# Performance work log

Hardware: AMD Instinct MI355X
Metric: run time of the kernel (lower is better)

Reference implementation:

```python
import jax, jax.numpy as jnp
import numpy as np

B = 16384       # batch size
NT = 26         # number of embedding tables
NROWS = 100000  # rows per table
M = 128         # embedding dim == bottom MLP output dim
BOT = [13, 512, 256, 128]
TOP = [479, 1024, 1024, 512, 256, 1]


def _linear_params(k, n, m):
    kw, kb = jax.random.split(k)
    W = jax.random.normal(kw, (m, n), jnp.float32) * np.sqrt(2.0 / (m + n))
    b = jax.random.normal(kb, (m,), jnp.float32) * np.sqrt(1.0 / m)
    return W, b


def setup_inputs() -> dict:
    key = jax.random.key(0)
    ks = jax.random.split(key, 16)
    dense_x = jax.random.normal(ks[0], (B, 13), jnp.float32)
    lS_i = jax.random.randint(ks[1], (NT, B), 0, NROWS, dtype=jnp.int32)
    lS_o = jnp.tile(jnp.arange(B, dtype=jnp.int32), (NT, 1))  # 1 index per bag
    s = float(np.sqrt(1.0 / NROWS))
    emb = jax.random.uniform(ks[2], (NT, NROWS, M), jnp.float32, -s, s)
    d = {"dense_x": dense_x, "lS_o": lS_o, "lS_i": lS_i, "emb": emb}
    for i in range(3):
        W, b = _linear_params(ks[3 + i], BOT[i], BOT[i + 1])
        d[f"bw{i}"] = W; d[f"bb{i}"] = b
    for i in range(5):
        W, b = _linear_params(ks[6 + i], TOP[i], TOP[i + 1])
        d[f"tw{i}"] = W; d[f"tb{i}"] = b
    return d


def _emb_bag_sum(table, idx, off):
    # nn.EmbeddingBag(mode='sum'): bag k sums rows idx[off[k]:off[k+1]]
    L = idx.shape[0]
    bag = jnp.searchsorted(off, jnp.arange(L, dtype=off.dtype), side='right') - 1
    return jax.ops.segment_sum(table[idx], bag, num_segments=B)  # [B, M]


def _forward(dense_x, emb, bws, bbs, tws, tbs, lS_o, lS_i):
    # bottom MLP (all ReLU, sigmoid_bot=-1)
    x = dense_x
    for W, b in zip(bws, bbs):
        x = jax.nn.relu(x @ W.T + b)
    # multi-table embedding-bag sum pooling
    ly = jax.vmap(_emb_bag_sum)(emb, lS_i, lS_o)          # [NT, B, M]
    # dot interaction
    T = jnp.concatenate([x[None], ly], axis=0).transpose(1, 0, 2)  # [B, NT+1, M]
    Z = jnp.einsum('bim,bjm->bij', T, T)                  # [B, 27, 27]
    li, lj = jnp.tril_indices(NT + 1, k=-1)               # pairs i>j, torch order
    Zflat = Z[:, li, lj]                                  # [B, 351]
    z = jnp.concatenate([x, Zflat], axis=1)               # [B, 479]
    # top MLP: ReLU except Sigmoid at layer index 4 (sigmoid_top=4)
    for i, (W, b) in enumerate(zip(tws, tbs)):
        z = z @ W.T + b
        z = jax.nn.sigmoid(z) if i == 4 else jax.nn.relu(z)
    return z


def reference(dense_x, lS_o, lS_i, emb,
              bw0, bb0, bw1, bb1, bw2, bb2,
              tw0, tb0, tw1, tb1, tw2, tb2, tw3, tb3, tw4, tb4):
    return _forward(dense_x, emb,
                    [bw0, bw1, bw2], [bb0, bb1, bb2],
                    [tw0, tw1, tw2, tw3, tw4], [tb0, tb1, tb2, tb3, tb4],
                    lS_o, lS_i)
```

## Files before the change

### kernel.cpp

```cpp
#include <hip/hip_runtime.h>
#include <cstdint>
#include <cstddef>

typedef _Float16 h16;
typedef __attribute__((ext_vector_type(8))) _Float16 half8;
typedef __attribute__((ext_vector_type(4))) _Float16 half4;
typedef __attribute__((ext_vector_type(2))) _Float16 half2v;
typedef __attribute__((ext_vector_type(4))) float f32x4;
typedef __attribute__((ext_vector_type(2))) float f32x2;

#define NB 16384
#define NTAB 26
#define NR 100000

__device__ __forceinline__ void gload16(const void* g, void* l) {
  __builtin_amdgcn_global_load_lds(
      (const __attribute__((address_space(1))) unsigned int*)g,
      (__attribute__((address_space(3))) unsigned int*)l, 16, 0, 0);
}

__global__ __launch_bounds__(256) void cvt_bot0_k(
    const float* __restrict__ s0, const float* __restrict__ s1,
    const float* __restrict__ s2, const float* __restrict__ s3,
    const float* __restrict__ s4, const float* __restrict__ s5,
    h16* __restrict__ dst, const float* __restrict__ x,
    const float* __restrict__ W0, const float* __restrict__ b0,
    h16* __restrict__ Y) {
  __shared__ float xs[32][14];
  int b = blockIdx.x;
  if (b >= 9344) {
    const int bb = b - 9344;
    const int row0 = bb * 32;
    const int tid = threadIdx.x;
    for (int i = tid; i < 32 * 13; i += 256) {
      int r = i / 13, k = i - r * 13;
      xs[r][k] = x[(size_t)(row0 + r) * 13 + k];
    }
    float w0[13], w1[13];
#pragma unroll
    for (int k = 0; k < 13; ++k) {
      w0[k] = W0[tid * 13 + k];
      w1[k] = W0[(tid + 256) * 13 + k];
    }
    const float bz0 = b0[tid], bz1 = b0[tid + 256];
    __syncthreads();
    for (int r = 0; r < 32; ++r) {
      float a0 = bz0, a1 = bz1;
#pragma unroll
      for (int k = 0; k < 13; ++k) {
        const float xv = xs[r][k];
        a0 += xv * w0[k];
        a1 += xv * w1[k];
      }
      Y[(size_t)(row0 + r) * 512 + tid] = (h16)fmaxf(a0, 0.f);
      Y[(size_t)(row0 + r) * 512 + tid + 256] = (h16)fmaxf(a1, 0.f);
    }
    return;
  }
  const float* src; int K, kl, i0; size_t doff;
  if (b < 512)       { src=s0; K=512;  kl=9;  i0=(b-0)*256;    doff=0; }
  else if (b < 640)  { src=s1; K=256;  kl=8;  i0=(b-512)*256;  doff=131072; }
  else if (b < 2688) { src=s2; K=479;  kl=9;  i0=(b-640)*256;  doff=163840; }
  else if (b < 6784) { src=s3; K=1024; kl=10; i0=(b-2688)*256; doff=688128; }
  else if (b < 8832) { src=s4; K=1024; kl=10; i0=(b-6784)*256; doff=1736704; }
  else               { src=s5; K=512;  kl=9;  i0=(b-8832)*256; doff=2260992; }
  int i = i0 + threadIdx.x;
  int n = i >> kl, k = i & ((1 << kl) - 1);
  dst[doff + i] = (k < K) ? (h16)src[(size_t)n * K + k] : (h16)0.f;
}

__global__ __launch_bounds__(256, 2) void mid_k(
    const h16* __restrict__ Y0, const h16* __restrict__ W1,
    const float* __restrict__ b1, const h16* __restrict__ W2,
    const float* __restrict__ b2, h16* __restrict__ Xc) {
  __shared__ __align__(16) h16 Sa[64 * 64];
  __shared__ __align__(16) h16 Sb[256 * 64];
  __shared__ __align__(16) h16 Y1[64 * 264];
  const int tid = threadIdx.x;
  const int lane = tid & 63;
  const int w = tid >> 6;
  const int l15 = lane & 15;
  const int kq = lane >> 4;
  const int l7 = lane & 7;
  const int lr8 = lane >> 3;
  const size_t row0 = (size_t)blockIdx.x * 64;

  const int sch = (lane & 7) ^ lr8;
  const h16* gA = Y0 + (row0 + w * 16 + lr8) * 512 + sch * 8;
  const h16* gB = W1 + ((size_t)w * 64 + lr8) * 512 + sch * 8;

  f32x4 acc[4][4] = {};
  for (int t = 0; t < 8; ++t) {
    const int k0 = t * 64;
#pragma unroll
    for (int i = 0; i < 2; ++i)
      gload16(gA + (size_t)i * 8 * 512 + k0, Sa + w * 1024 + i * 512);
#pragma unroll
    for (int i = 0; i < 8; ++i)
      gload16(gB + (size_t)i * 8 * 512 + k0, Sb + w * 4096 + i * 512);
    __syncthreads();
#pragma unroll
    for (int kk = 0; kk < 2; ++kk) {
      const int kb = kk * 4 + kq;
      half8 a[4], bfr[4];
#pragma unroll
      for (int mi = 0; mi < 4; ++mi)
        a[mi] = *(const half8*)&Sa[(mi * 16 + l15) * 64 + ((kb ^ l7) << 3)];
#pragma unroll
      for (int ni = 0; ni < 4; ++ni)
        bfr[ni] = *(const half8*)&Sb[(w * 64 + ni * 16 + l15) * 64 + ((kb ^ l7) << 3)];
#pragma unroll
      for (int mi = 0; mi < 4; ++mi)
#pragma unroll
        for (int ni = 0; ni < 4; ++ni)
          acc[mi][ni] = __builtin_amdgcn_mfma_f32_16x16x32_f16(bfr[ni], a[mi], acc[mi][ni], 0, 0, 0);
    }
    __syncthreads();
  }

#pragma unroll
  for (int mi = 0; mi < 4; ++mi) {
    const int row = mi * 16 + l15;
#pragma unroll
    for (int ni = 0; ni < 4; ++ni) {
      const int col = w * 64 + ni * 16 + kq * 4;
      const f32x4 bv = *(const f32x4*)&b1[col];
      half4 h;
#pragma unroll
      for (int ri = 0; ri < 4; ++ri)
        h[ri] = (h16)fmaxf(acc[mi][ni][ri] + bv[ri], 0.f);
      *(half4*)&Y1[row * 264 + col] = h;
    }
  }
  __syncthreads();

  f32x4 acc2[4][2] = {};
  for (int ks = 0; ks < 8; ++ks) {
    half8 av[4], bv[2];
#pragma unroll
    for (int mi = 0; mi < 4; ++mi)
      av[mi] = *(const half8*)&Y1[(mi * 16 + l15) * 264 + ks * 32 + kq * 8];
#pragma unroll
    for (int nf = 0; nf < 2; ++nf) {
      const int col = (w * 2 + nf) * 16 + l15;
      bv[nf] = *(const half8*)&W2[(size_t)col * 256 + ks * 32 + kq * 8];
    }
#pragma unroll
    for (int mi = 0; mi < 4; ++mi)
#pragma unroll
      for (int nf = 0; nf < 2; ++nf)
        acc2[mi][nf] = __builtin_amdgcn_mfma_f32_16x16x32_f16(bv[nf], av[mi], acc2[mi][nf], 0, 0, 0);
  }
#pragma unroll
  for (int mi = 0; mi < 4; ++mi) {
    const size_t row = row0 + mi * 16 + l15;
#pragma unroll
    for (int nf = 0; nf < 2; ++nf) {
      const int col = (w * 2 + nf) * 16 + kq * 4;
      const f32x4 bv = *(const f32x4*)&b2[col];
      half4 h;
#pragma unroll
      for (int ri = 0; ri < 4; ++ri)
        h[ri] = (h16)fmaxf(acc2[mi][nf][ri] + bv[ri], 0.f);
      *(half4*)&Xc[row * 128 + col] = h;
    }
  }
}

template <int GYL>
__global__ __launch_bounds__(256, 4) void gemm_sb(
    const h16* __restrict__ A, const h16* __restrict__ W,
    const float* __restrict__ bias, h16* __restrict__ C, int N, int K) {
  __shared__ __align__(16) h16 As[128 * 64];
  __shared__ __align__(16) h16 Bs[128 * 64];
  const int b = blockIdx.x;
  const int c8 = b & 7;
  const int q = b >> 3;
  const int jcol = q & ((1 << GYL) - 1);
  const int krow = ((q >> GYL) << 3) | c8;
  const int tid = threadIdx.x;
  const int lane = tid & 63;
  const int wave = tid >> 6;
  const int wm = wave >> 1, wn = wave & 1;
  const size_t row0 = (size_t)krow * 128;
  const size_t col0 = (size_t)jcol * 128;
  const int lr = lane >> 3;
  const int swzc = (((lane & 7) ^ lr) << 3);
  const int l15 = lane & 15;
  const int kq = lane >> 4;
  const int l7 = lane & 7;
  const int nt = K >> 6;

  const h16* ga = A + (row0 + wave * 32 + lr) * (size_t)K + swzc;
  const h16* gb = W + (col0 + wave * 32 + lr) * (size_t)K + swzc;

  f32x4 acc[4][4] = {};

  for (int t = 0; t < nt; ++t) {
    const int k0 = t << 6;
    h16* la = As + wave * 2048;
    h16* lb = Bs + wave * 2048;
#pragma unroll
    for (int i = 0; i < 4; ++i) {
      gload16(ga + (size_t)i * 8 * K + k0, la + i * 512);
      gload16(gb + (size_t)i * 8 * K + k0, lb + i * 512);
    }
    __syncthreads();
#pragma unroll
    for (int kk = 0; kk < 2; ++kk) {
      half8 a[4], bfr[4];
      const int kb = kk * 4 + kq;
#pragma unroll
      for (int mi = 0; mi < 4; ++mi)
        a[mi] = *(const half8*)&As[(wm * 64 + mi * 16 + l15) * 64 + ((kb ^ l7) << 3)];
#pragma unroll
      for (int ni = 0; ni < 4; ++ni)
        bfr[ni] = *(const half8*)&Bs[(wn * 64 + ni * 16 + l15) * 64 + ((kb ^ l7) << 3)];
#pragma unroll
      for (int mi = 0; mi < 4; ++mi)
#pragma unroll
        for (int ni = 0; ni < 4; ++ni)
          acc[mi][ni] = __builtin_amdgcn_mfma_f32_16x16x32_f16(a[mi], bfr[ni], acc[mi][ni], 0, 0, 0);
    }
    __syncthreads();
  }

#pragma unroll
  for (int mi = 0; mi < 4; ++mi)
#pragma unroll
    for (int ni = 0; ni < 4; ++ni) {
      const size_t col = col0 + wn * 64 + ni * 16 + l15;
      const float bv = bias[col];
#pragma unroll
      for (int ri = 0; ri < 4; ++ri) {
        const size_t row = row0 + wm * 64 + mi * 16 + kq * 4 + ri;
        float v = acc[mi][ni][ri] + bv;
        C[row * N + col] = (h16)fmaxf(v, 0.f);
      }
    }
}

__global__ __launch_bounds__(256, 4) void gemm_t3f(
    const h16* __restrict__ A, const h16* __restrict__ W,
    const float* __restrict__ bias, const float* __restrict__ w4,
    float* __restrict__ partial) {
  const int K = 512;
  __shared__ __align__(16) h16 As[128 * 64];
  __shared__ __align__(16) h16 Bs[128 * 64];
  const int b = blockIdx.x;
  const int c8 = b & 7;
  const int q = b >> 3;
  const int jcol = q & 1;
  const int krow = ((q >> 1) << 3) | c8;
  const int tid = threadIdx.x;
  const int lane = tid & 63;
  const int wave = tid >> 6;
  const int wm = wave >> 1, wn = wave & 1;
  const size_t row0 = (size_t)krow * 128;
  const size_t col0 = (size_t)jcol * 128;
  const int lr = lane >> 3;
  const int swzc = (((lane & 7) ^ lr) << 3);
  const int l15 = lane & 15;
  const int kq = lane >> 4;
  const int l7 = lane & 7;
  const int nt = K >> 6;

  const h16* ga = A + (row0 + wave * 32 + lr) * (size_t)K + swzc;
  const h16* gb = W + (col0 + wave * 32 + lr) * (size_t)K + swzc;

  f32x4 acc[4][4] = {};

  for (int t = 0; t < nt; ++t) {
    const int k0 = t << 6;
    h16* la = As + wave * 2048;
    h16* lb = Bs + wave * 2048;
#pragma unroll
    for (int i = 0; i < 4; ++i) {
      gload16(ga + (size_t)i * 8 * K + k0, la + i * 512);
      gload16(gb + (size_t)i * 8 * K + k0, lb + i * 512);
    }
    __syncthreads();
#pragma unroll
    for (int kk = 0; kk < 2; ++kk) {
      half8 a[4], bfr[4];
      const int kb = kk * 4 + kq;
#pragma unroll
      for (int mi = 0; mi < 4; ++mi)
        a[mi] = *(const half8*)&As[(wm * 64 + mi * 16 + l15) * 64 + ((kb ^ l7) << 3)];
#pragma unroll
      for (int ni = 0; ni < 4; ++ni)
        bfr[ni] = *(const half8*)&Bs[(wn * 64 + ni * 16 + l15) * 64 + ((kb ^ l7) << 3)];
#pragma unroll
      for (int mi = 0; mi < 4; ++mi)
#pragma unroll
        for (int ni = 0; ni < 4; ++ni)
          acc[mi][ni] = __builtin_amdgcn_mfma_f32_16x16x32_f16(a[mi], bfr[ni], acc[mi][ni], 0, 0, 0);
    }
    __syncthreads();
  }

  const int slot = jcol * 2 + wn;
#pragma unroll
  for (int mi = 0; mi < 4; ++mi) {
    float s[4] = {0.f, 0.f, 0.f, 0.f};
#pragma unroll
    for (int ni = 0; ni < 4; ++ni) {
      const size_t col = col0 + wn * 64 + ni * 16 + l15;
      const float bv = bias[col];
      const float wv = w4[col];
#pragma unroll
      for (int ri = 0; ri < 4; ++ri)
        s[ri] += fmaxf(acc[mi][ni][ri] + bv, 0.f) * wv;
    }
#pragma unroll
    for (int ri = 0; ri < 4; ++ri) {
      float v = s[ri];
      v += __shfl_xor(v, 1);
      v += __shfl_xor(v, 2);
      v += __shfl_xor(v, 4);
      v += __shfl_xor(v, 8);
      if (l15 == 0) {
        const size_t row = row0 + wm * 64 + mi * 16 + kq * 4 + ri;
        partial[(size_t)slot * NB + row] = v;
      }
    }
  }
}

__global__ __launch_bounds__(256) void sig_k(
    const float* __restrict__ partial, const float* __restrict__ bias,
    float* __restrict__ out) {
  int r = blockIdx.x * 256 + threadIdx.x;
  float v = partial[r] + partial[NB + r] + partial[2 * NB + r] +
            partial[3 * NB + r] + bias[0];
  out[r] = 1.f / (1.f + expf(-v));
}

__global__ __launch_bounds__(256) void interact_k(
    const h16* __restrict__ X, const float* __restrict__ emb,
    const int* __restrict__ lSi, h16* __restrict__ z) {
  __shared__ __align__(16) h16 T[4][32][136];
  const int lane = threadIdx.x & 63;
  const int wv = threadIdx.x >> 6;
  const size_t b = (size_t)blockIdx.x * 4 + wv;

  int idxs[NTAB];
#pragma unroll
  for (int t = 0; t < NTAB; ++t) idxs[t] = lSi[t * NB + (int)b];

  for (int i = lane; i < 5 * 128; i += 64)
    T[wv][27 + (i >> 7)][i & 127] = (h16)0.f;

  {
    half2v v = *(const half2v*)(X + b * 128 + lane * 2);
    *(half2v*)&T[wv][0][lane * 2] = v;
    *(half2v*)(z + b * 512 + lane * 2) = v;
  }
  const int thalf = lane >> 5;
  const int c4 = (lane & 31) * 4;
#pragma unroll
  for (int i = 0; i < NTAB / 2; ++i) {
    const int t = 2 * i + thalf;
    const f32x4 v = *(const f32x4*)(emb + ((size_t)t * NR + idxs[t]) * 128 + c4);
    half4 h;
#pragma unroll
    for (int j = 0; j < 4; ++j) h[j] = (h16)v[j];
    *(half4*)&T[wv][1 + t][c4] = h;
  }

  __syncthreads();

  f32x4 acc00 = {}, acc10 = {}, acc11 = {};
  const int l15 = lane & 15;
  const int kq = lane >> 4;
#pragma unroll
  for (int kk = 0; kk < 4; ++kk) {
    const int ko = kk * 32 + kq * 8;
    half8 a0 = *(const half8*)&T[wv][l15][ko];
    half8 a1 = *(const half8*)&T[wv][16 + l15][ko];
    acc00 = __builtin_amdgcn_mfma_f32_16x16x32_f16(a0, a0, acc00, 0, 0, 0);
    acc10 = __builtin_amdgcn_mfma_f32_16x16x32_f16(a1, a0, acc10, 0, 0, 0);
    acc11 = __builtin_amdgcn_mfma_f32_16x16x32_f16(a1, a1, acc11, 0, 0, 0);
  }
  h16* zr = z + b * 512 + 128;
#pragma unroll
  for (int ri = 0; ri < 4; ++ri) {
    int i0 = kq * 4 + ri;
    int i1 = 16 + i0;
    if (l15 < i0) zr[i0 * (i0 - 1) / 2 + l15] = (h16)acc00[ri];
    if (i1 < 27) {
      zr[i1 * (i1 - 1) / 2 + l15] = (h16)acc10[ri];
      int j1 = 16 + l15;
      if (j1 < i1) zr[i1 * (i1 - 1) / 2 + j1] = (h16)acc11[ri];
    }
  }
}

extern "C" void kernel_launch(void* const* d_in, const int* in_sizes, int n_in,
                              void* d_out, int out_size, void* d_ws, size_t ws_size,
                              hipStream_t stream) {
  const float* dense_x = (const float*)d_in[0];
  const int* lSi = (const int*)d_in[2];
  const float* emb = (const float*)d_in[3];
  const float* bw0 = (const float*)d_in[4];
  const float* bb0 = (const float*)d_in[5];
  const float* bw1 = (const float*)d_in[6];
  const float* bb1 = (const float*)d_in[7];
  const float* bw2 = (const float*)d_in[8];
  const float* bb2 = (const float*)d_in[9];
  const float* tw0 = (const float*)d_in[10];
  const float* tb0 = (const float*)d_in[11];
  const float* tw1 = (const float*)d_in[12];
  const float* tb1 = (const float*)d_in[13];
  const float* tw2 = (const float*)d_in[14];
  const float* tb2 = (const float*)d_in[15];
  const float* tw3 = (const float*)d_in[16];
  const float* tb3 = (const float*)d_in[17];
  const float* tw4 = (const float*)d_in[18];
  const float* tb4 = (const float*)d_in[19];
  float* out = (float*)d_out;

  char* ws = (char*)d_ws;
  const size_t MB = (size_t)1 << 20;
  h16* Y0 = (h16*)(ws + 0 * MB);
  h16* Xc = (h16*)(ws + 24 * MB);
  h16* Zz = (h16*)(ws + 32 * MB);
  h16* U0 = (h16*)(ws + 48 * MB);
  h16* U1 = (h16*)(ws + 0 * MB);
  h16* U2 = (h16*)(ws + 32 * MB);
  float* partial = (float*)(ws + 48 * MB);
  h16* w1p = (h16*)(ws + 80 * MB);
  h16* w2p = w1p + 256 * 512;
  h16* t0p = w2p + 128 * 256;
  h16* t1p = t0p + 1024 * 512;
  h16* t2p = t1p + 1024 * 1024;
  h16* t3p = t2p + 512 * 1024;
  (void)in_sizes; (void)n_in; (void)out_size; (void)ws_size;

  cvt_bot0_k<<<9344 + 512, 256, 0, stream>>>(bw1, bw2, tw0, tw1, tw2, tw3,
                                             w1p, dense_x, bw0, bb0, Y0);
  mid_k<<<256, 256, 0, stream>>>(Y0, w1p, bb1, w2p, bb2, Xc);
  interact_k<<<NB / 4, 256, 0, stream>>>(Xc, emb, lSi, Zz);
  gemm_sb<3><<<128 * 8, 256, 0, stream>>>(Zz, t0p, tb0, U0, 1024, 512);
  gemm_sb<3><<<128 * 8, 256, 0, stream>>>(U0, t1p, tb1, U1, 1024, 1024);
  gemm_sb<2><<<128 * 4, 256, 0, stream>>>(U1, t2p, tb2, U2, 512, 1024);
  gemm_t3f<<<128 * 2, 256, 0, stream>>>(U2, t3p, tb3, tw4, partial);
  sig_k<<<NB / 256, 256, 0, stream>>>(partial, tb4, out);
}
```

Baseline: 185.8 us.

## Halve row tiles in mid and final GEMMs, fuse sigmoid reduction into last GEMM

The bottom-MLP mid kernel and the last top-MLP GEMM now use 32-row blocks instead of 64/128-row tiles. This doubles the grid to 512 blocks so more of the GPU's CUs are busy. The final GEMM now covers all 256 output columns per block and reduces the dot with w4 across waves in shared memory. It applies bias and sigmoid in the same kernel, which removes the partial buffer and the separate sig_k launch. In exchange, each block reloads the full weight tile, so global and L2 weight traffic rises.

New measurement: 179.1 us. -3.6%, faster.

```diff
diff --git a/kernel.cpp b/kernel.cpp
--- a/kernel.cpp
+++ b/kernel.cpp
@@ -73,44 +73,43 @@
     const h16* __restrict__ Y0, const h16* __restrict__ W1,
     const float* __restrict__ b1, const h16* __restrict__ W2,
     const float* __restrict__ b2, h16* __restrict__ Xc) {
-  __shared__ __align__(16) h16 Sa[64 * 64];
+  __shared__ __align__(16) h16 Sa[32 * 64];
   __shared__ __align__(16) h16 Sb[256 * 64];
-  __shared__ __align__(16) h16 Y1[64 * 264];
+  __shared__ __align__(16) h16 Y1[32 * 264];
   const int tid = threadIdx.x;
   const int lane = tid & 63;
   const int w = tid >> 6;
   const int l15 = lane & 15;
   const int kq = lane >> 4;
   const int l7 = lane & 7;
-  const int lr8 = lane >> 3;
-  const size_t row0 = (size_t)blockIdx.x * 64;
-
-  const int sch = (lane & 7) ^ lr8;
-  const h16* gA = Y0 + (row0 + w * 16 + lr8) * 512 + sch * 8;
-  const h16* gB = W1 + ((size_t)w * 64 + lr8) * 512 + sch * 8;
-
-  f32x4 acc[4][4] = {};
+  const size_t row0 = (size_t)blockIdx.x * 32;
+
+  const int srow = tid >> 3;
+  const int sch = (tid & 7) ^ (srow & 7);
+  const h16* gA = Y0 + (row0 + srow) * 512 + sch * 8;
+  const h16* gB = W1 + (size_t)srow * 512 + sch * 8;
+
+  f32x4 acc[2][4] = {};
   for (int t = 0; t < 8; ++t) {
     const int k0 = t * 64;
-#pragma unroll
-    for (int i = 0; i < 2; ++i)
-      gload16(gA + (size_t)i * 8 * 512 + k0, Sa + w * 1024 + i * 512);
+    gload16(gA + k0, Sa + tid * 8);
 #pragma unroll
     for (int i = 0; i < 8; ++i)
-      gload16(gB + (size_t)i * 8 * 512 + k0, Sb + w * 4096 + i * 512);
+      gload16(gB + (size_t)(i * 32) * 512 + k0, Sb + i * 2048 + tid * 8);
     __syncthreads();
 #pragma unroll
     for (int kk = 0; kk < 2; ++kk) {
       const int kb = kk * 4 + kq;
-      half8 a[4], bfr[4];
-#pragma unroll
-      for (int mi = 0; mi < 4; ++mi)
-        a[mi] = *(const half8*)&Sa[(mi * 16 + l15) * 64 + ((kb ^ l7) << 3)];
+      const int sl = (kb ^ l7) << 3;
+      half8 a[2], bfr[4];
+#pragma unroll
+      for (int mi = 0; mi < 2; ++mi)
+        a[mi] = *(const half8*)&Sa[(mi * 16 + l15) * 64 + sl];
 #pragma unroll
       for (int ni = 0; ni < 4; ++ni)
-        bfr[ni] = *(const half8*)&Sb[(w * 64 + ni * 16 + l15) * 64 + ((kb ^ l7) << 3)];
-#pragma unroll
-      for (int mi = 0; mi < 4; ++mi)
+        bfr[ni] = *(const half8*)&Sb[(w * 64 + ni * 16 + l15) * 64 + sl];
+#pragma unroll
+      for (int mi = 0; mi < 2; ++mi)
 #pragma unroll
         for (int ni = 0; ni < 4; ++ni)
           acc[mi][ni] = __builtin_amdgcn_mfma_f32_16x16x32_f16(bfr[ni], a[mi], acc[mi][ni], 0, 0, 0);
@@ -119,7 +118,7 @@
   }
 
 #pragma unroll
-  for (int mi = 0; mi < 4; ++mi) {
+  for (int mi = 0; mi < 2; ++mi) {
     const int row = mi * 16 + l15;
 #pragma unroll
     for (int ni = 0; ni < 4; ++ni) {
@@ -134,11 +133,11 @@
   }
   __syncthreads();
 
-  f32x4 acc2[4][2] = {};
+  f32x4 acc2[2][2] = {};
   for (int ks = 0; ks < 8; ++ks) {
-    half8 av[4], bv[2];
-#pragma unroll
-    for (int mi = 0; mi < 4; ++mi)
+    half8 av[2], bv[2];
+#pragma unroll
+    for (int mi = 0; mi < 2; ++mi)
       av[mi] = *(const half8*)&Y1[(mi * 16 + l15) * 264 + ks * 32 + kq * 8];
 #pragma unroll
     for (int nf = 0; nf < 2; ++nf) {
@@ -146,13 +145,13 @@
       bv[nf] = *(const half8*)&W2[(size_t)col * 256 + ks * 32 + kq * 8];
     }
 #pragma unroll
-    for (int mi = 0; mi < 4; ++mi)
+    for (int mi = 0; mi < 2; ++mi)
 #pragma unroll
       for (int nf = 0; nf < 2; ++nf)
         acc2[mi][nf] = __builtin_amdgcn_mfma_f32_16x16x32_f16(bv[nf], av[mi], acc2[mi][nf], 0, 0, 0);
   }
 #pragma unroll
-  for (int mi = 0; mi < 4; ++mi) {
+  for (int mi = 0; mi < 2; ++mi) {
     const size_t row = row0 + mi * 16 + l15;
 #pragma unroll
     for (int nf = 0; nf < 2; ++nf) {
@@ -240,58 +239,48 @@
     }
 }
 
-__global__ __launch_bounds__(256, 4) void gemm_t3f(
+__global__ __launch_bounds__(256, 4) void gemm_t3s(
     const h16* __restrict__ A, const h16* __restrict__ W,
     const float* __restrict__ bias, const float* __restrict__ w4,
-    float* __restrict__ partial) {
+    const float* __restrict__ b4, float* __restrict__ out) {
   const int K = 512;
-  __shared__ __align__(16) h16 As[128 * 64];
-  __shared__ __align__(16) h16 Bs[128 * 64];
-  const int b = blockIdx.x;
-  const int c8 = b & 7;
-  const int q = b >> 3;
-  const int jcol = q & 1;
-  const int krow = ((q >> 1) << 3) | c8;
+  __shared__ __align__(16) h16 As[32 * 64];
+  __shared__ __align__(16) h16 Bs[256 * 64];
+  __shared__ float red[4][32];
   const int tid = threadIdx.x;
   const int lane = tid & 63;
-  const int wave = tid >> 6;
-  const int wm = wave >> 1, wn = wave & 1;
-  const size_t row0 = (size_t)krow * 128;
-  const size_t col0 = (size_t)jcol * 128;
-  const int lr = lane >> 3;
-  const int swzc = (((lane & 7) ^ lr) << 3);
+  const int w = tid >> 6;
   const int l15 = lane & 15;
   const int kq = lane >> 4;
   const int l7 = lane & 7;
-  const int nt = K >> 6;
-
-  const h16* ga = A + (row0 + wave * 32 + lr) * (size_t)K + swzc;
-  const h16* gb = W + (col0 + wave * 32 + lr) * (size_t)K + swzc;
-
-  f32x4 acc[4][4] = {};
-
-  for (int t = 0; t < nt; ++t) {
-    const int k0 = t << 6;
-    h16* la = As + wave * 2048;
-    h16* lb = Bs + wave * 2048;
-#pragma unroll
-    for (int i = 0; i < 4; ++i) {
-      gload16(ga + (size_t)i * 8 * K + k0, la + i * 512);
-      gload16(gb + (size_t)i * 8 * K + k0, lb + i * 512);
-    }
+  const size_t row0 = (size_t)blockIdx.x * 32;
+
+  const int srow = tid >> 3;
+  const int sch = (tid & 7) ^ (srow & 7);
+  const h16* gA = A + (row0 + srow) * (size_t)K + sch * 8;
+  const h16* gB = W + (size_t)srow * K + sch * 8;
+
+  f32x4 acc[2][4] = {};
+  for (int t = 0; t < 8; ++t) {
+    const int k0 = t * 64;
+    gload16(gA + k0, As + tid * 8);
+#pragma unroll
+    for (int i = 0; i < 8; ++i)
+      gload16(gB + (size_t)(i * 32) * K + k0, Bs + i * 2048 + tid * 8);
     __syncthreads();
 #pragma unroll
     for (int kk = 0; kk < 2; ++kk) {
-      half8 a[4], bfr[4];
       const int kb = kk * 4 + kq;
-#pragma unroll
-      for (int mi = 0; mi < 4; ++mi)
-        a[mi] = *(const half8*)&As[(wm * 64 + mi * 16 + l15) * 64 + ((kb ^ l7) << 3)];
+      const int sl = (kb ^ l7) << 3;
+      half8 a[2], bfr[4];
+#pragma unroll
+      for (int mi = 0; mi < 2; ++mi)
+        a[mi] = *(const half8*)&As[(mi * 16 + l15) * 64 + sl];
 #pragma unroll
       for (int ni = 0; ni < 4; ++ni)
-        bfr[ni] = *(const half8*)&Bs[(wn * 64 + ni * 16 + l15) * 64 + ((kb ^ l7) << 3)];
-#pragma unroll
-      for (int mi = 0; mi < 4; ++mi)
+        bfr[ni] = *(const half8*)&Bs[(w * 64 + ni * 16 + l15) * 64 + sl];
+#pragma unroll
+      for (int mi = 0; mi < 2; ++mi)
 #pragma unroll
         for (int ni = 0; ni < 4; ++ni)
           acc[mi][ni] = __builtin_amdgcn_mfma_f32_16x16x32_f16(a[mi], bfr[ni], acc[mi][ni], 0, 0, 0);
@@ -299,13 +288,12 @@
     __syncthreads();
   }
 
-  const int slot = jcol * 2 + wn;
-#pragma unroll
-  for (int mi = 0; mi < 4; ++mi) {
+#pragma unroll
+  for (int mi = 0; mi < 2; ++mi) {
     float s[4] = {0.f, 0.f, 0.f, 0.f};
 #pragma unroll
     for (int ni = 0; ni < 4; ++ni) {
-      const size_t col = col0 + wn * 64 + ni * 16 + l15;
+      const int col = w * 64 + ni * 16 + l15;
       const float bv = bias[col];
       const float wv = w4[col];
 #pragma unroll
@@ -319,21 +307,14 @@
       v += __shfl_xor(v, 2);
       v += __shfl_xor(v, 4);
       v += __shfl_xor(v, 8);
-      if (l15 == 0) {
-        const size_t row = row0 + wm * 64 + mi * 16 + kq * 4 + ri;
-        partial[(size_t)slot * NB + row] = v;
-      }
-    }
-  }
-}
-
-__global__ __launch_bounds__(256) void sig_k(
-    const float* __restrict__ partial, const float* __restrict__ bias,
-    float* __restrict__ out) {
-  int r = blockIdx.x * 256 + threadIdx.x;
-  float v = partial[r] + partial[NB + r] + partial[2 * NB + r] +
-            partial[3 * NB + r] + bias[0];
-  out[r] = 1.f / (1.f + expf(-v));
+      if (l15 == 0) red[w][mi * 16 + kq * 4 + ri] = v;
+    }
+  }
+  __syncthreads();
+  if (tid < 32) {
+    float v = red[0][tid] + red[1][tid] + red[2][tid] + red[3][tid] + b4[0];
+    out[row0 + tid] = 1.f / (1.f + expf(-v));
+  }
 }
 
 __global__ __launch_bounds__(256) void interact_k(
@@ -428,7 +409,6 @@
   h16* U0 = (h16*)(ws + 48 * MB);
   h16* U1 = (h16*)(ws + 0 * MB);
   h16* U2 = (h16*)(ws + 32 * MB);
-  float* partial = (float*)(ws + 48 * MB);
   h16* w1p = (h16*)(ws + 80 * MB);
   h16* w2p = w1p + 256 * 512;
   h16* t0p = w2p + 128 * 256;
@@ -439,11 +419,10 @@
 
   cvt_bot0_k<<<9344 + 512, 256, 0, stream>>>(bw1, bw2, tw0, tw1, tw2, tw3,
                                              w1p, dense_x, bw0, bb0, Y0);
-  mid_k<<<256, 256, 0, stream>>>(Y0, w1p, bb1, w2p, bb2, Xc);
+  mid_k<<<512, 256, 0, stream>>>(Y0, w1p, bb1, w2p, bb2, Xc);
   interact_k<<<NB / 4, 256, 0, stream>>>(Xc, emb, lSi, Zz);
   gemm_sb<3><<<128 * 8, 256, 0, stream>>>(Zz, t0p, tb0, U0, 1024, 512);
   gemm_sb<3><<<128 * 8, 256, 0, stream>>>(U0, t1p, tb1, U1, 1024, 1024);
   gemm_sb<2><<<128 * 4, 256, 0, stream>>>(U1, t2p, tb2, U2, 512, 1024);
-  gemm_t3f<<<128 * 2, 256, 0, stream>>>(U2, t3p, tb3, tw4, partial);
-  sig_k<<<NB / 256, 256, 0, stream>>>(partial, tb4, out);
-}
+  gemm_t3s<<<512, 256, 0, stream>>>(U2, t3p, tb3, tw4, tb4, out);
+}
```
